# Performance work log

Hardware: AMD Instinct MI355X
Metric: run time of the kernel (lower is better)

## Reference

```python
import jax, jax.numpy as jnp
import numpy as np

DT, TAU_S, TAU_M = 1.0, 4.0, 20.0
ALPHA = float(np.exp(-DT / TAU_S))   # synaptic current decay
BETA = float(np.exp(-DT / TAU_M))    # membrane potential decay
THRESH = 1.0
STEPS, BATCH, D1, D2 = 128, 256, 1024, 1024


def setup_inputs() -> dict:
    key = jax.random.key(0)
    k1, k2 = jax.random.split(key)
    inp = jax.random.uniform(k1, (STEPS, BATCH, D1), dtype=jnp.float32)
    # kaiming_normal_ on (d2, d1): std = sqrt(2 / fan_in), mu = 1.0
    weight = jax.random.normal(k2, (D2, D1), dtype=jnp.float32) * np.sqrt(2.0 / D1)
    return {"input": inp, "weight": weight}


def reference(input, weight):
    steps, batch = input.shape[0], input.shape[1]
    d2 = weight.shape[0]
    # Step i uses input[i-1]; precompute all linear projections at once.
    lin = jnp.einsum('tbi,oi->tbo', input[:-1], weight)  # [steps-1, B, d2]

    def step(carry, cur):
        syn, mem = carry
        # snntorch Synaptic, reset_mechanism='zero': reset from PREVIOUS mem
        reset = (mem > THRESH).astype(mem.dtype)
        syn = ALPHA * syn + cur
        mem = (BETA * mem + syn) * (1.0 - reset)
        spk = (mem > THRESH).astype(mem.dtype)
        return (syn, mem), (spk, mem, syn)

    init = (jnp.zeros((batch, d2), input.dtype), jnp.zeros((batch, d2), input.dtype))
    _, (spk, V, I) = jax.lax.scan(step, init, lin)
    z = jnp.zeros((1, batch, d2), input.dtype)  # step 0 stays zero
    output = jnp.concatenate([z, spk], axis=0)
    V = jnp.concatenate([z, V], axis=0)
    I = jnp.concatenate([z, I], axis=0)
    return output, V, I
```

## Files before the change

### kernel.cpp

```cpp
#include <hip/hip_runtime.h>
#include <hip/hip_fp16.h>


#define STEPS 128
#define BATCH 256
#define DIN   1024
#define DOUT  1024

#define ALPHA 0.7788007830714049f
#define BETA  0.9512294245007140f

constexpr int    GM      = (STEPS - 1) * BATCH;
constexpr size_t PLANE   = (size_t)BATCH * DOUT;
constexpr size_t A_ELEMS = (size_t)GM * DIN;
constexpr size_t W_ELEMS = (size_t)DOUT * DIN;

typedef __attribute__((ext_vector_type(8))) _Float16 half8;
typedef __attribute__((ext_vector_type(4))) float float4v;

__global__ __launch_bounds__(256)
void split_kernel(const float* __restrict__ x,
                  unsigned short* __restrict__ hi,
                  unsigned short* __restrict__ lo)
{
    const size_t i = (size_t)blockIdx.x * 256 + threadIdx.x;
    const float4 v = reinterpret_cast<const float4*>(x)[i];
    float f[4] = {v.x, v.y, v.z, v.w};
    unsigned short hb[4], lb[4];
#pragma unroll
    for (int j = 0; j < 4; ++j) {
        _Float16 h = (_Float16)f[j];
        _Float16 l = (_Float16)(f[j] - (float)h);
        hb[j] = *reinterpret_cast<unsigned short*>(&h);
        lb[j] = *reinterpret_cast<unsigned short*>(&l);
    }
    ushort4 hv = {hb[0], hb[1], hb[2], hb[3]};
    ushort4 lv = {lb[0], lb[1], lb[2], lb[3]};
    reinterpret_cast<ushort4*>(hi)[i] = hv;
    reinterpret_cast<ushort4*>(lo)[i] = lv;
}

__device__ __forceinline__ void load16(const unsigned short* g, unsigned short* l)
{
    __builtin_amdgcn_global_load_lds(
        (const __attribute__((address_space(1))) void*)g,
        (__attribute__((address_space(3))) void*)l, 16, 0, 0);
}

__global__ __launch_bounds__(256)
void gemm_kernel(const unsigned short* __restrict__ Ah,
                 const unsigned short* __restrict__ Al,
                 const unsigned short* __restrict__ Wh,
                 const unsigned short* __restrict__ Wl,
                 float* __restrict__ C)
{
    const int mt = blockIdx.x * 32 + (blockIdx.y >> 3);
    const int nt = blockIdx.y & 7;
    if (mt >= GM / 128) return;
    const int m0 = mt * 128;
    const int n0 = nt * 128;

    __shared__ __align__(16) unsigned short smem[4 * 4096];

    const int t    = threadIdx.x;
    const int wave = t >> 6, lane = t & 63;

    const int srow = t >> 2, skg = t & 3;
    const size_t offA = (size_t)(m0 + srow) * DIN + skg * 8;
    const size_t offB = (size_t)(n0 + srow) * DIN + skg * 8;
    unsigned short* lds0 = smem + (size_t)(wave * 64) * 8;
    unsigned short* lds1 = smem + (size_t)(256 + wave * 64) * 8;

    const int wr = wave >> 1, wc = wave & 1;
    const int lr = lane & 15, q = lane >> 4;

    float4v acc[4][4];
#pragma unroll
    for (int i = 0; i < 4; ++i)
#pragma unroll
        for (int j = 0; j < 4; ++j)
            acc[i][j] = (float4v){0.f, 0.f, 0.f, 0.f};

    for (int k0 = 0; k0 < DIN; k0 += 32) {
        const unsigned short* pAh = Ah + offA + k0;
        const unsigned short* pAl = Al + offA + k0;
        const unsigned short* pBh = Wh + offB + k0;
        const unsigned short* pBl = Wl + offB + k0;
        load16(pAh,            lds0);
        load16(pAh + 64 * DIN, lds1);
        load16(pAl,            lds0 + 4096);
        load16(pAl + 64 * DIN, lds1 + 4096);
        load16(pBh,            lds0 + 8192);
        load16(pBh + 64 * DIN, lds1 + 8192);
        load16(pBl,            lds0 + 12288);
        load16(pBl + 64 * DIN, lds1 + 12288);
        __syncthreads();

        half8 ah[4], al[4], bh[4], bl[4];
#pragma unroll
        for (int i = 0; i < 4; ++i) {
            const int r = wr * 64 + i * 16 + lr;
            ah[i] = *reinterpret_cast<const half8*>(smem +        r * 32 + q * 8);
            al[i] = *reinterpret_cast<const half8*>(smem + 4096 + r * 32 + q * 8);
        }
#pragma unroll
        for (int j = 0; j < 4; ++j) {
            const int r = wc * 64 + j * 16 + lr;
            bh[j] = *reinterpret_cast<const half8*>(smem + 8192  + r * 32 + q * 8);
            bl[j] = *reinterpret_cast<const half8*>(smem + 12288 + r * 32 + q * 8);
        }
#pragma unroll
        for (int i = 0; i < 4; ++i)
#pragma unroll
            for (int j = 0; j < 4; ++j) {
                acc[i][j] = __builtin_amdgcn_mfma_f32_16x16x32_f16(ah[i], bh[j], acc[i][j], 0, 0, 0);
                acc[i][j] = __builtin_amdgcn_mfma_f32_16x16x32_f16(ah[i], bl[j], acc[i][j], 0, 0, 0);
                acc[i][j] = __builtin_amdgcn_mfma_f32_16x16x32_f16(al[i], bh[j], acc[i][j], 0, 0, 0);
            }
        __syncthreads();
    }

#pragma unroll
    for (int i = 0; i < 4; ++i) {
        const int mrow = m0 + wr * 64 + i * 16 + q * 4;
#pragma unroll
        for (int j = 0; j < 4; ++j) {
            const int ncol = n0 + wc * 64 + j * 16 + lr;
#pragma unroll
            for (int rg = 0; rg < 4; ++rg)
                C[(size_t)(mrow + rg) * DOUT + ncol] = acc[i][j][rg];
        }
    }
}

__global__ __launch_bounds__(256)
void scan_kernel(float* __restrict__ out)
{
    const int idx = blockIdx.x * 256 + threadIdx.x;
    float* o0 = out;
    float* o1 = out + STEPS * PLANE;
    float* o2 = out + 2 * STEPS * PLANE;

    __builtin_nontemporal_store(0.0f, &o0[idx]);
    __builtin_nontemporal_store(0.0f, &o1[idx]);
    __builtin_nontemporal_store(0.0f, &o2[idx]);

    float n1 = o2[idx + PLANE];
    float n2 = o2[idx + 2 * PLANE];
    float n3 = o2[idx + 3 * PLANE];

    float syn = 0.0f, mem = 0.0f;
    size_t off = idx;
    for (int i = 1; i < STEPS; ++i) {
        off += PLANE;
        const float cur = n1; n1 = n2; n2 = n3;
        if (i + 3 < STEPS) n3 = o2[off + 3 * PLANE];
        const float reset = (mem > 1.0f) ? 1.0f : 0.0f;
        syn = ALPHA * syn + cur;
        mem = (BETA * mem + syn) * (1.0f - reset);
        const float spk = (mem > 1.0f) ? 1.0f : 0.0f;
        __builtin_nontemporal_store(spk, &o0[off]);
        __builtin_nontemporal_store(mem, &o1[off]);
        __builtin_nontemporal_store(syn, &o2[off]);
    }
}

extern "C" void kernel_launch(void* const* d_in, const int* in_sizes, int n_in,
                              void* d_out, int out_size, void* d_ws, size_t ws_size,
                              hipStream_t stream)
{
    const float* input  = (const float*)d_in[0];
    const float* weight = (const float*)d_in[1];
    float* out = (float*)d_out;

    unsigned short* Ah = (unsigned short*)out;
    unsigned short* Al = Ah + A_ELEMS;
    unsigned short* Wh = (unsigned short*)(out + STEPS * PLANE);
    unsigned short* Wl = Wh + W_ELEMS;
    float* lin = out + 2 * STEPS * PLANE + PLANE;

    split_kernel<<<(int)(A_ELEMS / 1024), 256, 0, stream>>>(input, Ah, Al);
    split_kernel<<<(int)(W_ELEMS / 1024), 256, 0, stream>>>(weight, Wh, Wl);

    gemm_kernel<<<dim3(8, 256), 256, 0, stream>>>(Ah, Al, Wh, Wl, lin);

    scan_kernel<<<(int)(PLANE / 256), 256, 0, stream>>>(out);
}
```

Baseline: 706.2 us.

## Rewrite split-fp16 GEMM with 256x256 tiles and 4-stage async LDS pipeline

Replaces the 128x128 single-buffered GEMM with a 512-thread, 256x256-tile kernel. It uses a 4-deep LDS ring buffer filled three stages ahead by direct global-to-LDS loads, with an XOR swizzle to avoid bank conflicts. The three hi/lo product passes become separate K phases of one long loop instead of three MFMAs per fragment, and blocks are mapped XCD-aware. This aims to hide global latency and raise operand reuse per load. The cost is higher register and LDS use, limiting occupancy to about one block per CU, plus a few redundant wrap-around prefetches at the end.

```diff
diff --git a/kernel.cpp b/kernel.cpp
--- a/kernel.cpp
+++ b/kernel.cpp
@@ -14,6 +14,8 @@
 constexpr size_t PLANE   = (size_t)BATCH * DOUT;
 constexpr size_t A_ELEMS = (size_t)GM * DIN;
 constexpr size_t W_ELEMS = (size_t)DOUT * DIN;
+
+constexpr int NKT = 96;
 
 typedef __attribute__((ext_vector_type(8))) _Float16 half8;
 typedef __attribute__((ext_vector_type(4))) float float4v;
@@ -47,90 +49,108 @@
         (__attribute__((address_space(3))) void*)l, 16, 0, 0);
 }
 
-__global__ __launch_bounds__(256)
+__global__ __launch_bounds__(512, 2)
 void gemm_kernel(const unsigned short* __restrict__ Ah,
                  const unsigned short* __restrict__ Al,
                  const unsigned short* __restrict__ Wh,
                  const unsigned short* __restrict__ Wl,
                  float* __restrict__ C)
 {
-    const int mt = blockIdx.x * 32 + (blockIdx.y >> 3);
-    const int nt = blockIdx.y & 7;
-    if (mt >= GM / 128) return;
-    const int m0 = mt * 128;
-    const int n0 = nt * 128;
-
-    __shared__ __align__(16) unsigned short smem[4 * 4096];
-
-    const int t    = threadIdx.x;
-    const int wave = t >> 6, lane = t & 63;
-
-    const int srow = t >> 2, skg = t & 3;
-    const size_t offA = (size_t)(m0 + srow) * DIN + skg * 8;
-    const size_t offB = (size_t)(n0 + srow) * DIN + skg * 8;
-    unsigned short* lds0 = smem + (size_t)(wave * 64) * 8;
-    unsigned short* lds1 = smem + (size_t)(256 + wave * 64) * 8;
-
-    const int wr = wave >> 1, wc = wave & 1;
-    const int lr = lane & 15, q = lane >> 4;
-
-    float4v acc[4][4];
-#pragma unroll
-    for (int i = 0; i < 4; ++i)
-#pragma unroll
-        for (int j = 0; j < 4; ++j)
-            acc[i][j] = (float4v){0.f, 0.f, 0.f, 0.f};
-
-    for (int k0 = 0; k0 < DIN; k0 += 32) {
-        const unsigned short* pAh = Ah + offA + k0;
-        const unsigned short* pAl = Al + offA + k0;
-        const unsigned short* pBh = Wh + offB + k0;
-        const unsigned short* pBl = Wl + offB + k0;
-        load16(pAh,            lds0);
-        load16(pAh + 64 * DIN, lds1);
-        load16(pAl,            lds0 + 4096);
-        load16(pAl + 64 * DIN, lds1 + 4096);
-        load16(pBh,            lds0 + 8192);
-        load16(pBh + 64 * DIN, lds1 + 8192);
-        load16(pBl,            lds0 + 12288);
-        load16(pBl + 64 * DIN, lds1 + 12288);
-        __syncthreads();
-
-        half8 ah[4], al[4], bh[4], bl[4];
-#pragma unroll
-        for (int i = 0; i < 4; ++i) {
-            const int r = wr * 64 + i * 16 + lr;
-            ah[i] = *reinterpret_cast<const half8*>(smem +        r * 32 + q * 8);
-            al[i] = *reinterpret_cast<const half8*>(smem + 4096 + r * 32 + q * 8);
-        }
-#pragma unroll
-        for (int j = 0; j < 4; ++j) {
-            const int r = wc * 64 + j * 16 + lr;
-            bh[j] = *reinterpret_cast<const half8*>(smem + 8192  + r * 32 + q * 8);
-            bl[j] = *reinterpret_cast<const half8*>(smem + 12288 + r * 32 + q * 8);
-        }
-#pragma unroll
-        for (int i = 0; i < 4; ++i)
-#pragma unroll
-            for (int j = 0; j < 4; ++j) {
-                acc[i][j] = __builtin_amdgcn_mfma_f32_16x16x32_f16(ah[i], bh[j], acc[i][j], 0, 0, 0);
-                acc[i][j] = __builtin_amdgcn_mfma_f32_16x16x32_f16(ah[i], bl[j], acc[i][j], 0, 0, 0);
-                acc[i][j] = __builtin_amdgcn_mfma_f32_16x16x32_f16(al[i], bh[j], acc[i][j], 0, 0, 0);
-            }
-        __syncthreads();
+    __shared__ __align__(16) unsigned short smem[65536];
+
+    const int lin = blockIdx.x;
+    const int xcd = lin & 7, slot = lin >> 3;
+    const int mp  = xcd * 16 + (slot >> 2);
+    const int nt  = slot & 3;
+    if (mp >= GM / 256) return;
+    const int m0 = mp * 256;
+    const int n0 = nt * 256;
+
+    const int t = threadIdx.x;
+    const int w = t >> 6, l = t & 63;
+    const int wr = w >> 2, wc = w & 3;
+    const int lr = l & 15, q = l >> 4;
+
+    const int swz = q ^ ((l >> 1) & 3);
+
+    const int laneA = (wr * 128 + lr) * 32 + swz * 8;
+    const int laneB = (wc * 64  + lr) * 32 + swz * 8;
+
+    const int srow = l >> 2;
+    const int sg   = ((l & 3) ^ ((l >> 3) & 3)) * 8;
+
+    const size_t sA0 = (size_t)(m0 + w * 32 +      srow) * DIN + sg;
+    const size_t sA1 = (size_t)(m0 + w * 32 + 16 + srow) * DIN + sg;
+    const size_t sB0 = (size_t)(n0 + w * 32 +      srow) * DIN + sg;
+    const size_t sB1 = (size_t)(n0 + w * 32 + 16 + srow) * DIN + sg;
+
+    unsigned short* dA0 = smem + w * 1024;
+    unsigned short* dA1 = smem + w * 1024 + 512;
+    unsigned short* dB0 = smem + 32768 + w * 1024;
+    unsigned short* dB1 = smem + 32768 + w * 1024 + 512;
+
+    auto STAGE = [&](int ks) {
+        const int p  = ks >> 5;
+        const int kk = (ks & 31) << 5;
+        const unsigned short* sa = (p == 1) ? Al : Ah;
+        const unsigned short* sw = (p == 2) ? Wl : Wh;
+        const int bo = (ks & 3) * 8192;
+        load16(sa + sA0 + kk, dA0 + bo);
+        load16(sa + sA1 + kk, dA1 + bo);
+        load16(sw + sB0 + kk, dB0 + bo);
+        load16(sw + sB1 + kk, dB1 + bo);
+    };
+
+    float4v acc[8][4];
+#pragma unroll
+    for (int m = 0; m < 8; ++m)
+#pragma unroll
+        for (int n = 0; n < 4; ++n)
+            acc[m][n] = (float4v){0.f, 0.f, 0.f, 0.f};
+
+    STAGE(0); STAGE(1); STAGE(2);
+    asm volatile("s_waitcnt vmcnt(8)" ::: "memory");
+    __builtin_amdgcn_s_barrier();
+
+    for (int kt = 0; kt < NKT; ++kt) {
+        const int bo = (kt & 3) * 8192;
+        const unsigned short* pA = smem + bo + laneA;
+        const unsigned short* pB = smem + 32768 + bo + laneB;
+
+        half8 a[8], b[4];
+#pragma unroll
+        for (int m = 0; m < 8; ++m)
+            a[m] = *reinterpret_cast<const half8*>(pA + m * 512);
+#pragma unroll
+        for (int n = 0; n < 4; ++n)
+            b[n] = *reinterpret_cast<const half8*>(pB + n * 512);
+
+        int ks = kt + 3;
+        if (ks >= NKT) ks -= NKT;
+        STAGE(ks);
+
+        __builtin_amdgcn_s_setprio(1);
+#pragma unroll
+        for (int m = 0; m < 8; ++m)
+#pragma unroll
+            for (int n = 0; n < 4; ++n)
+                acc[m][n] = __builtin_amdgcn_mfma_f32_16x16x32_f16(
+                    a[m], b[n], acc[m][n], 0, 0, 0);
+        __builtin_amdgcn_s_setprio(0);
+
+        asm volatile("s_waitcnt vmcnt(8)" ::: "memory");
+        __builtin_amdgcn_s_barrier();
     }
 
-#pragma unroll
-    for (int i = 0; i < 4; ++i) {
-        const int mrow = m0 + wr * 64 + i * 16 + q * 4;
-#pragma unroll
-        for (int j = 0; j < 4; ++j) {
-            const int ncol = n0 + wc * 64 + j * 16 + lr;
+    const int mw = m0 + wr * 128 + q * 4;
+    const int nw = n0 + wc * 64 + lr;
+#pragma unroll
+    for (int m = 0; m < 8; ++m)
+#pragma unroll
+        for (int n = 0; n < 4; ++n)
 #pragma unroll
             for (int rg = 0; rg < 4; ++rg)
-                C[(size_t)(mrow + rg) * DOUT + ncol] = acc[i][j][rg];
-        }
-    }
+                C[(size_t)(mw + m * 16 + rg) * DOUT + (nw + n * 16)] = acc[m][n][rg];
 }
 
 __global__ __launch_bounds__(256)
@@ -182,7 +202,7 @@
     split_kernel<<<(int)(A_ELEMS / 1024), 256, 0, stream>>>(input, Ah, Al);
     split_kernel<<<(int)(W_ELEMS / 1024), 256, 0, stream>>>(weight, Wh, Wl);
 
-    gemm_kernel<<<dim3(8, 256), 256, 0, stream>>>(Ah, Al, Wh, Wl, lin);
+    gemm_kernel<<<512, 512, 0, stream>>>(Ah, Al, Wh, Wl, lin);
 
     scan_kernel<<<(int)(PLANE / 256), 256, 0, stream>>>(out);
 }
```

Measured after the change: 690.2 us. -2.3%, faster.
